# Kernel tuning notes

Hardware: AMD Instinct MI355X
Metric: run time of the kernel (lower is better)

Reference implementation:

```python
import jax, jax.numpy as jnp
import numpy as np

N = 33554432  # number of samples


def setup_inputs() -> dict:
    key = jax.random.key(0)
    k1, k2 = jax.random.split(key)
    y = jax.random.normal(k1, (N,), dtype=jnp.float32)
    alpha = jax.random.uniform(k2, (N,), dtype=jnp.float32)
    return {"y": y, "alpha": alpha, "x_m": 1}


def reference(y, alpha, x_m):
    # Pareto NLL over entries with y > 0:
    #   loss = sum_{y>0} [ log(alpha)*x_m - (alpha+1)*log(y) ];  return -loss
    # Dynamic boolean indexing in torch becomes a static mask + jnp.where here.
    mask = y > 0
    safe_y = jnp.where(mask, y, 1.0)        # avoid log of non-positive values
    safe_a = jnp.where(mask, alpha, 1.0)    # avoid log(0) on masked-out entries
    terms = jnp.log(safe_a) * x_m - (safe_a + 1.0) * jnp.log(safe_y)
    loss = jnp.sum(jnp.where(mask, terms, 0.0))
    return -loss
```

## Files before the change

kernel.cpp:

```cpp
#include <hip/hip_runtime.h>

#define NBLOCKS 2048
#define NTHREADS 256

__global__ __launch_bounds__(NTHREADS) void pareto_partial(
    const float* __restrict__ y,
    const float* __restrict__ alpha,
    const int* __restrict__ xm_p,
    float* __restrict__ partials,
    int n)
{
    const float xm = (float)xm_p[0];
    const int n4 = n >> 2;
    const float4* __restrict__ y4 = (const float4*)y;
    const float4* __restrict__ a4 = (const float4*)alpha;

    float acc = 0.0f;
    const int stride = gridDim.x * blockDim.x;
    for (int i = blockIdx.x * blockDim.x + threadIdx.x; i < n4; i += stride) {
        float4 yv = y4[i];
        float4 av = a4[i];
        if (yv.x > 0.0f) acc += logf(av.x) * xm - (av.x + 1.0f) * logf(yv.x);
        if (yv.y > 0.0f) acc += logf(av.y) * xm - (av.y + 1.0f) * logf(yv.y);
        if (yv.z > 0.0f) acc += logf(av.z) * xm - (av.z + 1.0f) * logf(yv.z);
        if (yv.w > 0.0f) acc += logf(av.w) * xm - (av.w + 1.0f) * logf(yv.w);
    }

    if (blockIdx.x == 0 && threadIdx.x == 0) {
        for (int i = n4 << 2; i < n; ++i) {
            float yv = y[i];
            if (yv > 0.0f) {
                float av = alpha[i];
                acc += logf(av) * xm - (av + 1.0f) * logf(yv);
            }
        }
    }

    #pragma unroll
    for (int off = 32; off > 0; off >>= 1)
        acc += __shfl_down(acc, off, 64);

    __shared__ float wsum[NTHREADS / 64];
    const int lane = threadIdx.x & 63;
    const int wid  = threadIdx.x >> 6;
    if (lane == 0) wsum[wid] = acc;
    __syncthreads();
    if (threadIdx.x == 0) {
        float s = 0.0f;
        #pragma unroll
        for (int w = 0; w < NTHREADS / 64; ++w) s += wsum[w];
        partials[blockIdx.x] = s;
    }
}

__global__ __launch_bounds__(256) void pareto_final(
    const float* __restrict__ partials,
    float* __restrict__ out,
    int nb)
{
    double acc = 0.0;
    for (int i = threadIdx.x; i < nb; i += 256)
        acc += (double)partials[i];

    __shared__ double s[256];
    s[threadIdx.x] = acc;
    __syncthreads();
    #pragma unroll
    for (int off = 128; off > 0; off >>= 1) {
        if (threadIdx.x < off) s[threadIdx.x] += s[threadIdx.x + off];
        __syncthreads();
    }
    if (threadIdx.x == 0) out[0] = (float)(-s[0]);
}

extern "C" void kernel_launch(void* const* d_in, const int* in_sizes, int n_in,
                              void* d_out, int out_size, void* d_ws, size_t ws_size,
                              hipStream_t stream)
{
    const float* y     = (const float*)d_in[0];
    const float* alpha = (const float*)d_in[1];
    const int*   xm    = (const int*)d_in[2];
    float* out = (float*)d_out;
    float* partials = (float*)d_ws;

    const int n = in_sizes[0];
    int n4 = n >> 2;
    int grid = (n4 + NTHREADS - 1) / NTHREADS;
    if (grid > NBLOCKS) grid = NBLOCKS;
    if (grid < 1) grid = 1;

    pareto_partial<<<grid, NTHREADS, 0, stream>>>(y, alpha, xm, partials, n);
    pareto_final<<<1, 256, 0, stream>>>(partials, out, grid);
}
```

Baseline: 48.70 us.

## Fuse final reduction via last-block atomic counter, use fast log and 2x unroll

Merges the two-kernel reduction into one kernel in which the last block to finish, found through an atomic counter, sums the per-block partials. The main loop is unrolled by two with branchless selects and uses the __logf intrinsic instead of logf. This targets the second kernel launch and the cost of the math library log, but adds a memset launch, extra fences and atomics, and lower log accuracy.

After: 117.1 us. 140% more time.

```diff
diff --git a/kernel.cpp b/kernel.cpp
--- a/kernel.cpp
+++ b/kernel.cpp
@@ -1,13 +1,15 @@
 #include <hip/hip_runtime.h>
 
-#define NBLOCKS 2048
 #define NTHREADS 256
+#define MAXBLOCKS 2048
 
-__global__ __launch_bounds__(NTHREADS) void pareto_partial(
+__global__ __launch_bounds__(NTHREADS) void pareto_fused(
     const float* __restrict__ y,
     const float* __restrict__ alpha,
     const int* __restrict__ xm_p,
     float* __restrict__ partials,
+    unsigned int* __restrict__ counter,
+    float* __restrict__ out,
     int n)
 {
     const float xm = (float)xm_p[0];
@@ -17,21 +19,51 @@
 
     float acc = 0.0f;
     const int stride = gridDim.x * blockDim.x;
-    for (int i = blockIdx.x * blockDim.x + threadIdx.x; i < n4; i += stride) {
-        float4 yv = y4[i];
-        float4 av = a4[i];
-        if (yv.x > 0.0f) acc += logf(av.x) * xm - (av.x + 1.0f) * logf(yv.x);
-        if (yv.y > 0.0f) acc += logf(av.y) * xm - (av.y + 1.0f) * logf(yv.y);
-        if (yv.z > 0.0f) acc += logf(av.z) * xm - (av.z + 1.0f) * logf(yv.z);
-        if (yv.w > 0.0f) acc += logf(av.w) * xm - (av.w + 1.0f) * logf(yv.w);
+    int i = blockIdx.x * blockDim.x + threadIdx.x;
+
+    for (; i + stride < n4; i += 2 * stride) {
+        float4 ya = y4[i];
+        float4 aa = a4[i];
+        float4 yb = y4[i + stride];
+        float4 ab = a4[i + stride];
+
+        float t0 = __logf(aa.x) * xm - (aa.x + 1.0f) * __logf(ya.x);
+        float t1 = __logf(aa.y) * xm - (aa.y + 1.0f) * __logf(ya.y);
+        float t2 = __logf(aa.z) * xm - (aa.z + 1.0f) * __logf(ya.z);
+        float t3 = __logf(aa.w) * xm - (aa.w + 1.0f) * __logf(ya.w);
+        acc += (ya.x > 0.0f) ? t0 : 0.0f;
+        acc += (ya.y > 0.0f) ? t1 : 0.0f;
+        acc += (ya.z > 0.0f) ? t2 : 0.0f;
+        acc += (ya.w > 0.0f) ? t3 : 0.0f;
+
+        float u0 = __logf(ab.x) * xm - (ab.x + 1.0f) * __logf(yb.x);
+        float u1 = __logf(ab.y) * xm - (ab.y + 1.0f) * __logf(yb.y);
+        float u2 = __logf(ab.z) * xm - (ab.z + 1.0f) * __logf(yb.z);
+        float u3 = __logf(ab.w) * xm - (ab.w + 1.0f) * __logf(yb.w);
+        acc += (yb.x > 0.0f) ? u0 : 0.0f;
+        acc += (yb.y > 0.0f) ? u1 : 0.0f;
+        acc += (yb.z > 0.0f) ? u2 : 0.0f;
+        acc += (yb.w > 0.0f) ? u3 : 0.0f;
+    }
+    for (; i < n4; i += stride) {
+        float4 ya = y4[i];
+        float4 aa = a4[i];
+        float t0 = __logf(aa.x) * xm - (aa.x + 1.0f) * __logf(ya.x);
+        float t1 = __logf(aa.y) * xm - (aa.y + 1.0f) * __logf(ya.y);
+        float t2 = __logf(aa.z) * xm - (aa.z + 1.0f) * __logf(ya.z);
+        float t3 = __logf(aa.w) * xm - (aa.w + 1.0f) * __logf(ya.w);
+        acc += (ya.x > 0.0f) ? t0 : 0.0f;
+        acc += (ya.y > 0.0f) ? t1 : 0.0f;
+        acc += (ya.z > 0.0f) ? t2 : 0.0f;
+        acc += (ya.w > 0.0f) ? t3 : 0.0f;
     }
 
     if (blockIdx.x == 0 && threadIdx.x == 0) {
-        for (int i = n4 << 2; i < n; ++i) {
-            float yv = y[i];
+        for (int j = n4 << 2; j < n; ++j) {
+            float yv = y[j];
             if (yv > 0.0f) {
-                float av = alpha[i];
-                acc += logf(av) * xm - (av + 1.0f) * logf(yv);
+                float av = alpha[j];
+                acc += __logf(av) * xm - (av + 1.0f) * __logf(yv);
             }
         }
     }
@@ -41,36 +73,38 @@
         acc += __shfl_down(acc, off, 64);
 
     __shared__ float wsum[NTHREADS / 64];
+    __shared__ int isLast;
     const int lane = threadIdx.x & 63;
     const int wid  = threadIdx.x >> 6;
     if (lane == 0) wsum[wid] = acc;
     __syncthreads();
+
     if (threadIdx.x == 0) {
         float s = 0.0f;
         #pragma unroll
         for (int w = 0; w < NTHREADS / 64; ++w) s += wsum[w];
         partials[blockIdx.x] = s;
+        __threadfence();
+        unsigned int t = atomicAdd(counter, 1u);
+        isLast = (t == gridDim.x - 1) ? 1 : 0;
     }
-}
+    __syncthreads();
 
-__global__ __launch_bounds__(256) void pareto_final(
-    const float* __restrict__ partials,
-    float* __restrict__ out,
-    int nb)
-{
-    double acc = 0.0;
-    for (int i = threadIdx.x; i < nb; i += 256)
-        acc += (double)partials[i];
-
-    __shared__ double s[256];
-    s[threadIdx.x] = acc;
-    __syncthreads();
-    #pragma unroll
-    for (int off = 128; off > 0; off >>= 1) {
-        if (threadIdx.x < off) s[threadIdx.x] += s[threadIdx.x + off];
+    if (isLast) {
+        __threadfence();
+        double d = 0.0;
+        for (int j = threadIdx.x; j < (int)gridDim.x; j += NTHREADS)
+            d += (double)partials[j];
+        __shared__ double ds[NTHREADS];
+        ds[threadIdx.x] = d;
         __syncthreads();
+        #pragma unroll
+        for (int off = NTHREADS / 2; off > 0; off >>= 1) {
+            if (threadIdx.x < off) ds[threadIdx.x] += ds[threadIdx.x + off];
+            __syncthreads();
+        }
+        if (threadIdx.x == 0) out[0] = (float)(-ds[0]);
     }
-    if (threadIdx.x == 0) out[0] = (float)(-s[0]);
 }
 
 extern "C" void kernel_launch(void* const* d_in, const int* in_sizes, int n_in,
@@ -81,14 +115,16 @@
     const float* alpha = (const float*)d_in[1];
     const int*   xm    = (const int*)d_in[2];
     float* out = (float*)d_out;
+
     float* partials = (float*)d_ws;
+    unsigned int* counter = (unsigned int*)((char*)d_ws + MAXBLOCKS * sizeof(float));
 
     const int n = in_sizes[0];
     int n4 = n >> 2;
     int grid = (n4 + NTHREADS - 1) / NTHREADS;
-    if (grid > NBLOCKS) grid = NBLOCKS;
+    if (grid > MAXBLOCKS) grid = MAXBLOCKS;
     if (grid < 1) grid = 1;
 
-    pareto_partial<<<grid, NTHREADS, 0, stream>>>(y, alpha, xm, partials, n);
-    pareto_final<<<1, 256, 0, stream>>>(partials, out, grid);
+    hipMemsetAsync(counter, 0, sizeof(unsigned int), stream);
+    pareto_fused<<<grid, NTHREADS, 0, stream>>>(y, alpha, xm, partials, counter, out, n);
 }
```
